# Kernel optimization log

Measured on AMD Instinct MI355X. Metric: run time of the kernel, lower is better.

The kernel has to match this reference:

```python
import jax, jax.numpy as jnp
import numpy as np

N = 80000; E = 1280000; IN = 128; H1 = 128; H2 = 128; H3 = 64
L1D = 512; L2D = 256; OUT = 10; K = 2; GROUP = 40


def setup_inputs() -> dict:
    key = jax.random.key(0)
    ks = jax.random.split(key, 16)
    s = 0.05
    d = {}
    d['x'] = jax.random.normal(ks[0], (N, IN), jnp.float32)
    d['edge_index'] = jax.random.randint(ks[1], (2, E), 0, N, jnp.int32)
    # SGConv linears (applied after K-hop propagation)
    d['W1'] = jax.random.normal(ks[2], (H1, IN), jnp.float32) * s
    d['b1'] = jnp.zeros((H1,), jnp.float32)
    d['W2'] = jax.random.normal(ks[3], (H2, H1), jnp.float32) * s
    d['b2'] = jnp.zeros((H2,), jnp.float32)
    # GATConv (heads=1)
    d['Wg'] = jax.random.normal(ks[4], (H3, H2), jnp.float32) * s
    d['att_src'] = jax.random.normal(ks[5], (H3,), jnp.float32) * s
    d['att_dst'] = jax.random.normal(ks[6], (H3,), jnp.float32) * s
    d['bg'] = jnp.zeros((H3,), jnp.float32)
    # MLP head
    d['L1'] = jax.random.normal(ks[7], (L1D, H3 * GROUP), jnp.float32) * s
    d['bl1'] = jnp.zeros((L1D,), jnp.float32)
    d['L2'] = jax.random.normal(ks[8], (L2D, L1D), jnp.float32) * s
    d['bl2'] = jnp.zeros((L2D,), jnp.float32)
    d['L3'] = jax.random.normal(ks[9], (OUT, L2D), jnp.float32) * s
    d['bl3'] = jnp.zeros((OUT,), jnp.float32)
    return d


def _lrelu(v, slope=0.1):
    return jnp.where(v > 0, v, slope * v)


def _forward(x, src, dst, norm, W1, b1, W2, b2, Wg, bg, att_src, att_dst,
             L1, bl1, L2, bl2, L3, bl3):
    # SGConv: x <- S^K x, then linear. S = D^-1/2 (A+I) D^-1/2
    def prop(h):
        return jax.ops.segment_sum(norm[:, None] * h[src], dst, num_segments=N)

    h = x
    for _ in range(K):
        h = prop(h)
    h = _lrelu(h @ W1.T + b1)
    for _ in range(K):
        h = prop(h)
    h = _lrelu(h @ W2.T + b2)

    # GATConv (1 head), self-loops included in (src, dst)
    g = h @ Wg.T                                   # [N, H3]
    a_s = g @ att_src                              # [N]
    a_d = g @ att_dst                              # [N]
    e = _lrelu(a_s[src] + a_d[dst], 0.2)           # [E+N]
    emax = jax.ops.segment_max(e, dst, num_segments=N)
    ee = jnp.exp(e - emax[dst])
    den = jax.ops.segment_sum(ee, dst, num_segments=N)
    alpha = ee / den[dst]
    h = jax.ops.segment_sum(alpha[:, None] * g[src], dst, num_segments=N) + bg
    h = _lrelu(h)

    # pool 40-node groups, MLP head
    h = h.reshape(N // GROUP, H3 * GROUP)
    h = _lrelu(h @ L1.T + bl1)
    h = _lrelu(h @ L2.T + bl2)
    h = _lrelu(h @ L3.T + bl3)
    return h


def reference(x, edge_index, W1, b1, W2, b2, Wg, bg, att_src, att_dst,
              L1, bl1, L2, bl2, L3, bl3):
    loops = jnp.arange(N, dtype=edge_index.dtype)
    src = jnp.concatenate([edge_index[0], loops])
    dst = jnp.concatenate([edge_index[1], loops])
    deg = jax.ops.segment_sum(jnp.ones_like(src, jnp.float32), dst, num_segments=N)
    dinv = jnp.where(deg > 0, jax.lax.rsqrt(deg), 0.0)
    norm = dinv[src] * dinv[dst]
    return _forward(x, src, dst, norm, W1, b1, W2, b2, Wg, bg, att_src,
                    att_dst, L1, bl1, L2, bl2, L3, bl3)
```

## Files before the change

kernel.cpp:

```cpp
#include <hip/hip_runtime.h>

#define N_NODES 80000
#define N_EDGES 1280000
#define NNZ (N_EDGES + N_NODES)
#define DIM 128
#define HD3 64
#define GROUP 40
#define NPOOL (N_NODES / GROUP)
#define L1DIM 512
#define L2DIM 256
#define OUTD 10
#define SPLITK 4
#define L1K (HD3 * GROUP)

#define NB_BUCKETS ((N_NODES + 255) >> 8)
#define NB_PAD 320
#define EPB 8192
#define NBLK ((NNZ + EPB - 1) / EPB)

#define QX  (N_NODES * DIM / 4)
#define QW1 (DIM * DIM / 4)
#define QW2 (DIM * DIM / 4)
#define QWG (HD3 * DIM / 4)
#define QL1 (L1DIM * L1K / 4)
#define QTOT (QX + QW1 + QW2 + QWG + QL1)

typedef unsigned int u32;
typedef unsigned short u16;
typedef __bf16 bf16x8 __attribute__((ext_vector_type(8)));
typedef float f32x4 __attribute__((ext_vector_type(4)));
typedef float f32x2 __attribute__((ext_vector_type(2)));

__device__ __forceinline__ float lrelu(float v, float s) { return v > 0.f ? v : s * v; }

__device__ __forceinline__ float b2f(u16 b) {
    u32 u = ((u32)b) << 16;
    float f; __builtin_memcpy(&f, &u, 4); return f;
}
__device__ __forceinline__ u16 f2b(float f) {
    u32 u; __builtin_memcpy(&u, &f, 4);
    return (u16)((u + 0x7fffu + ((u >> 16) & 1u)) >> 16);
}
__device__ __forceinline__ f32x2 bf2(u32 v) {
    f32x2 r;
    r.x = __uint_as_float(v << 16);
    r.y = __uint_as_float(v & 0xffff0000u);
    return r;
}


__global__ __launch_bounds__(256) void k_hist(const int* __restrict__ ei, u32* __restrict__ cnt) {
    __shared__ u32 h[NB_PAD];
    for (int i = threadIdx.x; i < NB_PAD; i += 256) h[i] = 0;
    __syncthreads();
    int base = blockIdx.x * EPB;
    #pragma unroll 4
    for (int i = 0; i < EPB / 256; ++i) {
        int idx = base + i * 256 + threadIdx.x;
        if (idx < NNZ) {
            int d = (idx < N_EDGES) ? ei[N_EDGES + idx] : idx - N_EDGES;
            atomicAdd(&h[d >> 8], 1u);
        }
    }
    __syncthreads();
    for (int b = threadIdx.x; b < NB_BUCKETS; b += 256)
        cnt[blockIdx.x * NB_PAD + b] = h[b];
}

__global__ __launch_bounds__(256) void k_bscan_col(const u32* __restrict__ cnt,
                                                   u32* __restrict__ basep,
                                                   u32* __restrict__ btot) {
    int b = blockIdx.x, t = threadIdx.x;
    u32 v = (t < NBLK) ? cnt[t * NB_PAD + b] : 0;
    __shared__ u32 sm[256];
    sm[t] = v; __syncthreads();
    for (int off = 1; off < 256; off <<= 1) {
        u32 u = (t >= off) ? sm[t - off] : 0; __syncthreads();
        sm[t] += u; __syncthreads();
    }
    if (t < NBLK) basep[t * NB_PAD + b] = sm[t] - v;
    if (t == 255) btot[b] = sm[255];
}

__global__ __launch_bounds__(512) void k_bscan_top(const u32* __restrict__ btot,
                                                   u32* __restrict__ bbase,
                                                   int* __restrict__ row_ptr) {
    __shared__ u32 sm[512];
    int t = threadIdx.x;
    u32 v = (t < NB_BUCKETS) ? btot[t] : 0;
    sm[t] = v; __syncthreads();
    for (int off = 1; off < 512; off <<= 1) {
        u32 u = (t >= off) ? sm[t - off] : 0; __syncthreads();
        sm[t] += u; __syncthreads();
    }
    if (t < NB_BUCKETS) bbase[t] = sm[t] - v;
    if (t == NB_BUCKETS - 1) bbase[NB_BUCKETS] = sm[t];
    if (t == 0) row_ptr[N_NODES] = NNZ;
}

__global__ __launch_bounds__(256) void k_binscatter(const int* __restrict__ ei,
                                                    const u32* __restrict__ basep,
                                                    const u32* __restrict__ bbase,
                                                    u32* __restrict__ pairs) {
    __shared__ u32 rk[NB_PAD];
    for (int i = threadIdx.x; i < NB_PAD; i += 256) rk[i] = 0;
    __syncthreads();
    int base = blockIdx.x * EPB;
    #pragma unroll 4
    for (int i = 0; i < EPB / 256; ++i) {
        int idx = base + i * 256 + threadIdx.x;
        if (idx < NNZ) {
            int s, d;
            if (idx < N_EDGES) { s = ei[idx]; d = ei[N_EDGES + idx]; }
            else { s = idx - N_EDGES; d = s; }
            int b = d >> 8;
            u32 r = atomicAdd(&rk[b], 1u);
            u32 pos = bbase[b] + basep[blockIdx.x * NB_PAD + b] + r;
            pairs[pos] = ((u32)(d & 255) << 24) | (u32)s;
        }
    }
}

__global__ __launch_bounds__(256) void k_build_csr(const u32* __restrict__ pairs,
                                                   const u32* __restrict__ bbase,
                                                   int* __restrict__ row_ptr,
                                                   float* __restrict__ dinv,
                                                   int* __restrict__ col_src) {
    __shared__ u32 c[256], sc[256], ex[256];
    int t = threadIdx.x, b = blockIdx.x;
    int lo = bbase[b], hi = bbase[b + 1];
    c[t] = 0;
    __syncthreads();
    for (int i = lo + t; i < hi; i += 256)
        atomicAdd(&c[pairs[i] >> 24], 1u);
    __syncthreads();
    u32 cv = c[t];
    sc[t] = cv;
    __syncthreads();
    for (int off = 1; off < 256; off <<= 1) {
        u32 u = (t >= off) ? sc[t - off] : 0; __syncthreads();
        sc[t] += u; __syncthreads();
    }
    ex[t] = sc[t] - cv;
    int node = (b << 8) + t;
    if (node < N_NODES) {
        row_ptr[node] = lo + (int)ex[t];
        dinv[node] = rsqrtf((float)cv);
    }
    c[t] = 0;
    __syncthreads();
    for (int i = lo + t; i < hi; i += 256) {
        u32 p = pairs[i];
        u32 dl = p >> 24;
        u32 r = atomicAdd(&c[dl], 1u);
        col_src[lo + (int)ex[dl] + (int)r] = (int)(p & 0xFFFFFFu);
    }
}


__global__ __launch_bounds__(256) void k_f2b_all(const float* __restrict__ x,   u16* __restrict__ xb,
                                                 const float* __restrict__ w1,  u16* __restrict__ w1b,
                                                 const float* __restrict__ w2,  u16* __restrict__ w2b,
                                                 const float* __restrict__ wg,  u16* __restrict__ wgb,
                                                 const float* __restrict__ l1,  u16* __restrict__ l1b) {
    int i = blockIdx.x * blockDim.x + threadIdx.x;
    const float* src; u16* dst; int off;
    if (i < QX)                        { src = x;  dst = xb;  off = i; }
    else if (i < QX + QW1)             { src = w1; dst = w1b; off = i - QX; }
    else if (i < QX + QW1 + QW2)       { src = w2; dst = w2b; off = i - QX - QW1; }
    else if (i < QX + QW1 + QW2 + QWG) { src = wg; dst = wgb; off = i - QX - QW1 - QW2; }
    else if (i < QTOT)                 { src = l1; dst = l1b; off = i - QX - QW1 - QW2 - QWG; }
    else return;
    float4 v = ((const float4*)src)[off];
    ushort4 o = { f2b(v.x), f2b(v.y), f2b(v.z), f2b(v.w) };
    ((ushort4*)dst)[off] = o;
}


__global__ __launch_bounds__(256) void k_prop_bf(const int* __restrict__ row_ptr,
                                                 const int* __restrict__ col_src,
                                                 const float* __restrict__ dinv,
                                                 const u16* __restrict__ hin,
                                                 u16* __restrict__ hout) {
    int lane = threadIdx.x & 63;
    int node = blockIdx.x * 4 + (threadIdx.x >> 6);
    if (node >= N_NODES) return;
    int j0 = row_ptr[node], j1 = row_ptr[node + 1];
    float dn = dinv[node];
    const int grp = lane >> 4;
    const int dl  = lane & 15;
    f32x2 acc[4] = {};

    for (int base = j0; base < j1; base += 64) {
        int cnt = j1 - base; if (cnt > 64) cnt = 64;
        int jj = base + lane;
        int sidx = (jj < j1) ? col_src[jj] : 0;
        int l = 0;
        for (; l + 16 <= cnt; l += 16) {
            uint4 v[4]; f32x2 w2[4];
            #pragma unroll
            for (int q = 0; q < 4; ++q) {
                int s = __shfl(sidx, l + q * 4 + grp);
                float wq = dinv[s] * dn;
                w2[q].x = wq; w2[q].y = wq;
                v[q] = *(const uint4*)(hin + (size_t)s * DIM + dl * 8);
            }
            #pragma unroll
            for (int q = 0; q < 4; ++q) {
                acc[0] = __builtin_elementwise_fma(bf2(v[q].x), w2[q], acc[0]);
                acc[1] = __builtin_elementwise_fma(bf2(v[q].y), w2[q], acc[1]);
                acc[2] = __builtin_elementwise_fma(bf2(v[q].z), w2[q], acc[2]);
                acc[3] = __builtin_elementwise_fma(bf2(v[q].w), w2[q], acc[3]);
            }
        }
        for (; l + 4 <= cnt; l += 4) {
            int s = __shfl(sidx, l + grp);
            float wq = dinv[s] * dn;
            f32x2 w2; w2.x = wq; w2.y = wq;
            uint4 v = *(const uint4*)(hin + (size_t)s * DIM + dl * 8);
            acc[0] = __builtin_elementwise_fma(bf2(v.x), w2, acc[0]);
            acc[1] = __builtin_elementwise_fma(bf2(v.y), w2, acc[1]);
            acc[2] = __builtin_elementwise_fma(bf2(v.z), w2, acc[2]);
            acc[3] = __builtin_elementwise_fma(bf2(v.w), w2, acc[3]);
        }
        for (; l < cnt; ++l) {
            int s = __shfl(sidx, l);
            if (grp == 0) {
                float wq = dinv[s] * dn;
                f32x2 w2; w2.x = wq; w2.y = wq;
                uint4 v = *(const uint4*)(hin + (size_t)s * DIM + dl * 8);
                acc[0] = __builtin_elementwise_fma(bf2(v.x), w2, acc[0]);
                acc[1] = __builtin_elementwise_fma(bf2(v.y), w2, acc[1]);
                acc[2] = __builtin_elementwise_fma(bf2(v.z), w2, acc[2]);
                acc[3] = __builtin_elementwise_fma(bf2(v.w), w2, acc[3]);
            }
        }
    }
    #pragma unroll
    for (int d = 0; d < 4; ++d) {
        acc[d].x += __shfl_xor(acc[d].x, 16); acc[d].x += __shfl_xor(acc[d].x, 32);
        acc[d].y += __shfl_xor(acc[d].y, 16); acc[d].y += __shfl_xor(acc[d].y, 32);
    }
    if (grp == 0) {
        uint4 o;
        o.x = (u32)f2b(acc[0].x) | ((u32)f2b(acc[0].y) << 16);
        o.y = (u32)f2b(acc[1].x) | ((u32)f2b(acc[1].y) << 16);
        o.z = (u32)f2b(acc[2].x) | ((u32)f2b(acc[2].y) << 16);
        o.w = (u32)f2b(acc[3].x) | ((u32)f2b(acc[3].y) << 16);
        *(uint4*)(hout + (size_t)node * DIM + dl * 8) = o;
    }
}


template<int NT, bool BIAS, bool ACT, bool ATTN>
__global__ __launch_bounds__(256) void k_gemm_mfma(const u16* __restrict__ A,
                                                   const u16* __restrict__ Wb,
                                                   const float* __restrict__ b,
                                                   u16* __restrict__ C,
                                                   const float* __restrict__ att_src,
                                                   const float* __restrict__ att_dst,
                                                   float* __restrict__ a_s,
                                                   float* __restrict__ a_d,
                                                   int M, int K) {
    const int lane = threadIdx.x & 63;
    const int wave = threadIdx.x >> 6;
    const int m0 = blockIdx.x * 64 + wave * 16;
    const int row = lane & 15, kg = lane >> 4;
    const int Ntot = NT * 16;

    const u16* Ap = A + (size_t)(m0 + row) * K + kg * 8;
    f32x4 acc[NT] = {};

    for (int k0 = 0; k0 < K; k0 += 32) {
        bf16x8 a = *(const bf16x8*)(Ap + k0);
        #pragma unroll
        for (int nt = 0; nt < NT; ++nt) {
            const u16* Wp = Wb + (size_t)(nt * 16 + row) * K + k0 + kg * 8;
            bf16x8 bb = *(const bf16x8*)Wp;
            acc[nt] = __builtin_amdgcn_mfma_f32_16x16x32_bf16(a, bb, acc[nt], 0, 0, 0);
        }
    }

    #pragma unroll
    for (int nt = 0; nt < NT; ++nt) {
        float bias = BIAS ? b[nt * 16 + row] : 0.f;
        #pragma unroll
        for (int r = 0; r < 4; ++r) {
            float v = acc[nt][r] + bias;
            if (ACT) v = lrelu(v, 0.1f);
            int crow = m0 + kg * 4 + r;
            C[(size_t)crow * Ntot + nt * 16 + row] = f2b(v);
        }
    }

    if (ATTN) {
        float s1[4] = {}, s2[4] = {};
        #pragma unroll
        for (int nt = 0; nt < NT; ++nt) {
            float as = att_src[nt * 16 + row];
            float av = att_dst[nt * 16 + row];
            #pragma unroll
            for (int r = 0; r < 4; ++r) {
                s1[r] += acc[nt][r] * as;
                s2[r] += acc[nt][r] * av;
            }
        }
        #pragma unroll
        for (int r = 0; r < 4; ++r) {
            #pragma unroll
            for (int off = 1; off < 16; off <<= 1) {
                s1[r] += __shfl_xor(s1[r], off);
                s2[r] += __shfl_xor(s2[r], off);
            }
        }
        if (row == 0) {
            #pragma unroll
            for (int r = 0; r < 4; ++r) {
                a_s[m0 + kg * 4 + r] = s1[r];
                a_d[m0 + kg * 4 + r] = s2[r];
            }
        }
    }
}


template<int NT>
__global__ __launch_bounds__(256) void k_gemm_mfma_sk(const u16* __restrict__ A,
                                                      const u16* __restrict__ Wb,
                                                      float* __restrict__ C,
                                                      int M, int Ntot, int K, int kChunk) {
    const int lane = threadIdx.x & 63;
    const int wave = threadIdx.x >> 6;
    const int m0 = blockIdx.x * 64 + wave * 16;
    const int row = lane & 15, kg = lane >> 4;
    const int n0 = blockIdx.y * NT * 16;
    const int kBeg = blockIdx.z * kChunk;

    int arow = m0 + row; if (arow >= M) arow = M - 1;
    const u16* Ap = A + (size_t)arow * K + kg * 8;
    f32x4 acc[NT] = {};

    for (int k0 = kBeg; k0 < kBeg + kChunk; k0 += 32) {
        bf16x8 a = *(const bf16x8*)(Ap + k0);
        #pragma unroll
        for (int nt = 0; nt < NT; ++nt) {
            const u16* Wp = Wb + (size_t)(n0 + nt * 16 + row) * K + k0 + kg * 8;
            bf16x8 bb = *(const bf16x8*)Wp;
            acc[nt] = __builtin_amdgcn_mfma_f32_16x16x32_bf16(a, bb, acc[nt], 0, 0, 0);
        }
    }

    float* Cp = C + (size_t)blockIdx.z * M * Ntot;
    #pragma unroll
    for (int nt = 0; nt < NT; ++nt) {
        #pragma unroll
        for (int r = 0; r < 4; ++r) {
            int crow = m0 + kg * 4 + r;
            if (crow < M) Cp[(size_t)crow * Ntot + n0 + nt * 16 + row] = acc[nt][r];
        }
    }
}


template<int BM, int BN, int BK, int TM, int TN, bool BIAS, bool ACT>
__global__ __launch_bounds__(256) void k_gemm(const float* __restrict__ A,
                                              const float* __restrict__ W,
                                              const float* __restrict__ b,
                                              float* __restrict__ C,
                                              int M, int Ntot, int K) {
    __shared__ float As[BK][BM + 4];
    __shared__ float Bs[BK][BN + 4];
    const int t = threadIdx.x;
    const int m0 = blockIdx.x * BM, n0 = blockIdx.y * BN;
    const int ty = t / (BN / TN), tx = t % (BN / TN);

    float acc[TM][TN] = {};

    for (int k0 = 0; k0 < K; k0 += BK) {
        #pragma unroll
        for (int p = 0; p < BM * BK / 4 / 256; ++p) {
            int id = p * 256 + t;
            int m = id % BM, kk = (id / BM) * 4;
            float4 v = {0.f, 0.f, 0.f, 0.f};
            if (m0 + m < M) v = *(const float4*)(A + (size_t)(m0 + m) * K + k0 + kk);
            As[kk + 0][m] = v.x; As[kk + 1][m] = v.y;
            As[kk + 2][m] = v.z; As[kk + 3][m] = v.w;
        }
        #pragma unroll
        for (int p = 0; p < BN * BK / 4 / 256; ++p) {
            int id = p * 256 + t;
            int n = id % BN, kk = (id / BN) * 4;
            float4 v = *(const float4*)(W + (size_t)(n0 + n) * K + k0 + kk);
            Bs[kk + 0][n] = v.x; Bs[kk + 1][n] = v.y;
            Bs[kk + 2][n] = v.z; Bs[kk + 3][n] = v.w;
        }
        __syncthreads();

        #pragma unroll
        for (int k = 0; k < BK; ++k) {
            float a[TM], bb[TN];
            #pragma unroll
            for (int i = 0; i < TM; ++i) a[i] = As[k][ty * TM + i];
            #pragma unroll
            for (int j = 0; j < TN; ++j) bb[j] = Bs[k][tx * TN + j];
            #pragma unroll
            for (int i = 0; i < TM; ++i)
                #pragma unroll
                for (int j = 0; j < TN; ++j)
                    acc[i][j] += a[i] * bb[j];
        }
        __syncthreads();
    }

    #pragma unroll
    for (int i = 0; i < TM; ++i) {
        int row = m0 + ty * TM + i;
        if (row >= M) continue;
        float4 o;
        float* op = (float*)&o;
        #pragma unroll
        for (int j = 0; j < TN; ++j) {
            float r = acc[i][j];
            if (BIAS) r += b[n0 + tx * TN + j];
            if (ACT) r = lrelu(r, 0.1f);
            op[j] = r;
        }
        *(float4*)(C + (size_t)row * Ntot + n0 + tx * TN) = o;
    }
}

__global__ __launch_bounds__(256) void k_splitk_reduce(const float* __restrict__ part,
                                                       const float* __restrict__ b,
                                                       float* __restrict__ out) {
    const int total4 = NPOOL * L1DIM / 4;
    int idx = blockIdx.x * blockDim.x + threadIdx.x;
    if (idx >= total4) return;
    const size_t stride4 = (size_t)NPOOL * L1DIM / 4;
    const float4* p4 = (const float4*)part;
    float4 s = p4[idx];
    #pragma unroll
    for (int z = 1; z < SPLITK; ++z) {
        float4 v = p4[idx + z * stride4];
        s.x += v.x; s.y += v.y; s.z += v.z; s.w += v.w;
    }
    int col = (idx * 4) % L1DIM;
    float4 bb = *(const float4*)(b + col);
    s.x = lrelu(s.x + bb.x, 0.1f); s.y = lrelu(s.y + bb.y, 0.1f);
    s.z = lrelu(s.z + bb.z, 0.1f); s.w = lrelu(s.w + bb.w, 0.1f);
    ((float4*)out)[idx] = s;
}


template<int KD, int OD, bool BIAS, bool ACT>
__global__ void k_linear(const float* __restrict__ in, const float* __restrict__ W,
                         const float* __restrict__ b, float* __restrict__ out, int nrows) {
    int idx = blockIdx.x * blockDim.x + threadIdx.x;
    int n = idx / OD, o = idx % OD;
    if (n >= nrows) return;
    const float4* ar = (const float4*)(in + (size_t)n * KD);
    const float4* wr = (const float4*)(W + (size_t)o * KD);
    float4 acc = {0.f, 0.f, 0.f, 0.f};
    #pragma unroll 8
    for (int k = 0; k < KD / 4; ++k) {
        float4 a = ar[k], w = wr[k];
        acc.x += a.x * w.x; acc.y += a.y * w.y;
        acc.z += a.z * w.z; acc.w += a.w * w.w;
    }
    float r = (acc.x + acc.y) + (acc.z + acc.w);
    if (BIAS) r += b[o];
    if (ACT) r = lrelu(r, 0.1f);
    out[idx] = r;
}


__global__ __launch_bounds__(256) void k_gat(const int* __restrict__ row_ptr,
                                             const int* __restrict__ col_src,
                                             const u16* __restrict__ g,
                                             const float* __restrict__ a_s,
                                             const float* __restrict__ a_d,
                                             const float* __restrict__ bg,
                                             u16* __restrict__ hout) {
    __shared__ float wbuf[4][64];
    int lane = threadIdx.x & 63;
    int wid  = threadIdx.x >> 6;
    int node = blockIdx.x * 4 + wid;
    if (node >= N_NODES) return;
    int j0 = row_ptr[node], j1 = row_ptr[node + 1];
    float ad = a_d[node];
    const int grp = lane >> 4, dl = lane & 15;
    float m = -1e30f, den = 0.f;
    f32x2 acc[2] = {};

    for (int base = j0; base < j1; base += 64) {
        int cnt = j1 - base; if (cnt > 64) cnt = 64;
        int jj = base + lane;
        int sidx = 0;
        float e = -1e30f;
        if (jj < j1) { sidx = col_src[jj]; e = lrelu(a_s[sidx] + ad, 0.2f); }
        float cm = e;
        for (int off = 32; off; off >>= 1) cm = fmaxf(cm, __shfl_xor(cm, off));
        float nm = fmaxf(m, cm);
        float scale = __expf(m - nm);
        float wv = (jj < j1) ? __expf(e - nm) : 0.f;
        wbuf[wid][lane] = wv;
        float cden = wv;
        for (int off = 32; off; off >>= 1) cden += __shfl_xor(cden, off);
        den = den * scale + cden;
        f32x2 sc2; sc2.x = scale; sc2.y = scale;
        acc[0] *= sc2; acc[1] *= sc2;
        m = nm;
        int l = 0;
        for (; l + 16 <= cnt; l += 16) {
            uint2 v[4]; f32x2 w2[4];
            #pragma unroll
            for (int q = 0; q < 4; ++q) {
                int e2 = l + q * 4 + grp;
                int s = __shfl(sidx, e2);
                float wq = wbuf[wid][e2];
                w2[q].x = wq; w2[q].y = wq;
                v[q] = *(const uint2*)(g + (size_t)s * HD3 + dl * 4);
            }
            #pragma unroll
            for (int q = 0; q < 4; ++q) {
                acc[0] = __builtin_elementwise_fma(bf2(v[q].x), w2[q], acc[0]);
                acc[1] = __builtin_elementwise_fma(bf2(v[q].y), w2[q], acc[1]);
            }
        }
        for (; l + 4 <= cnt; l += 4) {
            int e2 = l + grp;
            int s = __shfl(sidx, e2);
            float wq = wbuf[wid][e2];
            f32x2 w2; w2.x = wq; w2.y = wq;
            uint2 v = *(const uint2*)(g + (size_t)s * HD3 + dl * 4);
            acc[0] = __builtin_elementwise_fma(bf2(v.x), w2, acc[0]);
            acc[1] = __builtin_elementwise_fma(bf2(v.y), w2, acc[1]);
        }
        for (; l < cnt; ++l) {
            int s = __shfl(sidx, l);
            if (grp == 0) {
                float wq = wbuf[wid][l];
                f32x2 w2; w2.x = wq; w2.y = wq;
                uint2 v = *(const uint2*)(g + (size_t)s * HD3 + dl * 4);
                acc[0] = __builtin_elementwise_fma(bf2(v.x), w2, acc[0]);
                acc[1] = __builtin_elementwise_fma(bf2(v.y), w2, acc[1]);
            }
        }
    }
    #pragma unroll
    for (int d = 0; d < 2; ++d) {
        acc[d].x += __shfl_xor(acc[d].x, 16); acc[d].x += __shfl_xor(acc[d].x, 32);
        acc[d].y += __shfl_xor(acc[d].y, 16); acc[d].y += __shfl_xor(acc[d].y, 32);
    }
    if (grp == 0) {
        float r0 = lrelu(acc[0].x / den + bg[dl * 4 + 0], 0.1f);
        float r1 = lrelu(acc[0].y / den + bg[dl * 4 + 1], 0.1f);
        float r2 = lrelu(acc[1].x / den + bg[dl * 4 + 2], 0.1f);
        float r3 = lrelu(acc[1].y / den + bg[dl * 4 + 3], 0.1f);
        uint2 o;
        o.x = (u32)f2b(r0) | ((u32)f2b(r1) << 16);
        o.y = (u32)f2b(r2) | ((u32)f2b(r3) << 16);
        *(uint2*)(hout + (size_t)node * HD3 + dl * 4) = o;
    }
}


extern "C" void kernel_launch(void* const* d_in, const int* in_sizes, int n_in,
                              void* d_out, int out_size, void* d_ws, size_t ws_size,
                              hipStream_t stream) {
    const float* x   = (const float*)d_in[0];
    const int*   ei  = (const int*)d_in[1];
    const float* W1  = (const float*)d_in[2];
    const float* b1  = (const float*)d_in[3];
    const float* W2  = (const float*)d_in[4];
    const float* b2  = (const float*)d_in[5];
    const float* Wg  = (const float*)d_in[6];
    const float* att_src = (const float*)d_in[7];
    const float* att_dst = (const float*)d_in[8];
    const float* bg  = (const float*)d_in[9];
    const float* L1  = (const float*)d_in[10];
    const float* bl1 = (const float*)d_in[11];
    const float* L2  = (const float*)d_in[12];
    const float* bl2 = (const float*)d_in[13];
    const float* L3  = (const float*)d_in[14];
    const float* bl3 = (const float*)d_in[15];
    float* out = (float*)d_out;

    char* w = (char*)d_ws;
    auto alloc = [&](size_t bytes) {
        char* p = w;
        w += (bytes + 255) & ~(size_t)255;
        return p;
    };
    int*   row_ptr  = (int*)alloc((size_t)(N_NODES + 1) * 4);
    float* dinv     = (float*)alloc((size_t)N_NODES * 4);
    int*   col_src  = (int*)alloc((size_t)NNZ * 4);
    u32*   pairs    = (u32*)alloc((size_t)NNZ * 4);
    u32*   cnt      = (u32*)alloc((size_t)NBLK * NB_PAD * 4);
    u32*   basep    = (u32*)alloc((size_t)NBLK * NB_PAD * 4);
    u32*   btot     = (u32*)alloc((size_t)NB_PAD * 4);
    u32*   bbase    = (u32*)alloc((size_t)(NB_BUCKETS + 1) * 4);
    u16*   bufX     = (u16*)alloc((size_t)N_NODES * DIM * 2);
    u16*   bufA     = (u16*)alloc((size_t)N_NODES * DIM * 2);
    u16*   bufB     = (u16*)alloc((size_t)N_NODES * DIM * 2);
    float* a_s      = (float*)alloc((size_t)N_NODES * 4);
    float* a_d      = (float*)alloc((size_t)N_NODES * 4);
    float* p1       = (float*)alloc((size_t)NPOOL * L1DIM * 4);
    float* p2       = (float*)alloc((size_t)NPOOL * L2DIM * 4);
    u16*   W1b      = (u16*)alloc((size_t)DIM * DIM * 2);
    u16*   W2b      = (u16*)alloc((size_t)DIM * DIM * 2);
    u16*   Wgb      = (u16*)alloc((size_t)HD3 * DIM * 2);
    u16*   L1b      = (u16*)alloc((size_t)L1DIM * L1K * 2);
    u16*   gb    = bufX;
    u16*   hGb   = bufA;
    float* skbuf = (float*)bufB;

    dim3 b256(256);
    k_hist<<<NBLK, b256, 0, stream>>>(ei, cnt);
    k_bscan_col<<<NB_BUCKETS, b256, 0, stream>>>(cnt, basep, btot);
    k_bscan_top<<<1, 512, 0, stream>>>(btot, bbase, row_ptr);
    k_binscatter<<<NBLK, b256, 0, stream>>>(ei, basep, bbase, pairs);
    k_build_csr<<<NB_BUCKETS, b256, 0, stream>>>(pairs, bbase, row_ptr, dinv, col_src);

    k_f2b_all<<<(QTOT + 255) / 256, b256, 0, stream>>>(x, bufX, W1, W1b, W2, W2b, Wg, Wgb, L1, L1b);

    int nb = (N_NODES + 3) / 4;
    int gemm_nb = N_NODES / 64;
    k_prop_bf<<<nb, b256, 0, stream>>>(row_ptr, col_src, dinv, bufX, bufA);
    k_prop_bf<<<nb, b256, 0, stream>>>(row_ptr, col_src, dinv, bufA, bufB);
    k_gemm_mfma<8, true, true, false><<<gemm_nb, b256, 0, stream>>>(
        bufB, W1b, b1, bufA, nullptr, nullptr, nullptr, nullptr, N_NODES, DIM);
    k_prop_bf<<<nb, b256, 0, stream>>>(row_ptr, col_src, dinv, bufA, bufB);
    k_prop_bf<<<nb, b256, 0, stream>>>(row_ptr, col_src, dinv, bufB, bufA);
    k_gemm_mfma<8, true, true, false><<<gemm_nb, b256, 0, stream>>>(
        bufA, W2b, b2, bufB, nullptr, nullptr, nullptr, nullptr, N_NODES, DIM);
    k_gemm_mfma<4, false, false, true><<<gemm_nb, b256, 0, stream>>>(
        bufB, Wgb, nullptr, gb, att_src, att_dst, a_s, a_d, N_NODES, DIM);
    k_gat<<<nb, b256, 0, stream>>>(row_ptr, col_src, gb, a_s, a_d, bg, hGb);
    k_gemm_mfma_sk<8><<<dim3(32, 4, SPLITK), b256, 0, stream>>>(
        hGb, L1b, skbuf, NPOOL, L1DIM, L1K, L1K / SPLITK);
    k_splitk_reduce<<<(NPOOL * L1DIM / 4 + 255) / 256, b256, 0, stream>>>(skbuf, bl1, p1);
    k_gemm<64, 64, 32, 4, 4, true, true><<<dim3(32, 4), b256, 0, stream>>>(p1, L2, bl2, p2, NPOOL, L2DIM, L1DIM);
    k_linear<256, 10, true, true><<<(NPOOL * 10 + 255) / 256, b256, 0, stream>>>(p2, L3, bl3, out, NPOOL);
}
```

Baseline: 473.2 us.

## Apply linear layers before propagation and fuse bias/activation into propagation epilogue

```diff
diff --git a/kernel.cpp b/kernel.cpp
--- a/kernel.cpp
+++ b/kernel.cpp
@@ -18,12 +18,12 @@
 #define EPB 8192
 #define NBLK ((NNZ + EPB - 1) / EPB)
 
-#define QX  (N_NODES * DIM / 4)
 #define QW1 (DIM * DIM / 4)
 #define QW2 (DIM * DIM / 4)
 #define QWG (HD3 * DIM / 4)
 #define QL1 (L1DIM * L1K / 4)
-#define QTOT (QX + QW1 + QW2 + QWG + QL1)
+#define QWTOT (QW1 + QW2 + QWG + QL1)
+#define F2B_NB ((QWTOT + 255) / 256)
 
 typedef unsigned int u32;
 typedef unsigned short u16;
@@ -47,10 +47,33 @@
     r.y = __uint_as_float(v & 0xffff0000u);
     return r;
 }
-
-
-__global__ __launch_bounds__(256) void k_hist(const int* __restrict__ ei, u32* __restrict__ cnt) {
+__device__ __forceinline__ bf16x8 pack8(float4 f0, float4 f1) {
+    union { bf16x8 v; u16 s[8]; } u;
+    u.s[0] = f2b(f0.x); u.s[1] = f2b(f0.y); u.s[2] = f2b(f0.z); u.s[3] = f2b(f0.w);
+    u.s[4] = f2b(f1.x); u.s[5] = f2b(f1.y); u.s[6] = f2b(f1.z); u.s[7] = f2b(f1.w);
+    return u.v;
+}
+
+
+__global__ __launch_bounds__(256) void k_hist(const int* __restrict__ ei, u32* __restrict__ cnt,
+                                              const float* __restrict__ w1, u16* __restrict__ w1b,
+                                              const float* __restrict__ w2, u16* __restrict__ w2b,
+                                              const float* __restrict__ wg, u16* __restrict__ wgb,
+                                              const float* __restrict__ l1, u16* __restrict__ l1b) {
     __shared__ u32 h[NB_PAD];
+    if (blockIdx.x >= NBLK) {
+        int i = (blockIdx.x - NBLK) * 256 + threadIdx.x;
+        const float* src; u16* dst; int off;
+        if (i < QW1)                   { src = w1; dst = w1b; off = i; }
+        else if (i < QW1 + QW2)        { src = w2; dst = w2b; off = i - QW1; }
+        else if (i < QW1 + QW2 + QWG)  { src = wg; dst = wgb; off = i - QW1 - QW2; }
+        else if (i < QWTOT)            { src = l1; dst = l1b; off = i - QW1 - QW2 - QWG; }
+        else return;
+        float4 v = ((const float4*)src)[off];
+        ushort4 o = { f2b(v.x), f2b(v.y), f2b(v.z), f2b(v.w) };
+        ((ushort4*)dst)[off] = o;
+        return;
+    }
     for (int i = threadIdx.x; i < NB_PAD; i += 256) h[i] = 0;
     __syncthreads();
     int base = blockIdx.x * EPB;
@@ -158,30 +181,13 @@
 }
 
 
-__global__ __launch_bounds__(256) void k_f2b_all(const float* __restrict__ x,   u16* __restrict__ xb,
-                                                 const float* __restrict__ w1,  u16* __restrict__ w1b,
-                                                 const float* __restrict__ w2,  u16* __restrict__ w2b,
-                                                 const float* __restrict__ wg,  u16* __restrict__ wgb,
-                                                 const float* __restrict__ l1,  u16* __restrict__ l1b) {
-    int i = blockIdx.x * blockDim.x + threadIdx.x;
-    const float* src; u16* dst; int off;
-    if (i < QX)                        { src = x;  dst = xb;  off = i; }
-    else if (i < QX + QW1)             { src = w1; dst = w1b; off = i - QX; }
-    else if (i < QX + QW1 + QW2)       { src = w2; dst = w2b; off = i - QX - QW1; }
-    else if (i < QX + QW1 + QW2 + QWG) { src = wg; dst = wgb; off = i - QX - QW1 - QW2; }
-    else if (i < QTOT)                 { src = l1; dst = l1b; off = i - QX - QW1 - QW2 - QWG; }
-    else return;
-    float4 v = ((const float4*)src)[off];
-    ushort4 o = { f2b(v.x), f2b(v.y), f2b(v.z), f2b(v.w) };
-    ((ushort4*)dst)[off] = o;
-}
-
-
+template<bool EPI>
 __global__ __launch_bounds__(256) void k_prop_bf(const int* __restrict__ row_ptr,
                                                  const int* __restrict__ col_src,
                                                  const float* __restrict__ dinv,
                                                  const u16* __restrict__ hin,
-                                                 u16* __restrict__ hout) {
+                                                 u16* __restrict__ hout,
+                                                 const float* __restrict__ bias) {
     int lane = threadIdx.x & 63;
     int node = blockIdx.x * 4 + (threadIdx.x >> 6);
     if (node >= N_NODES) return;
@@ -242,6 +248,14 @@
         acc[d].y += __shfl_xor(acc[d].y, 16); acc[d].y += __shfl_xor(acc[d].y, 32);
     }
     if (grp == 0) {
+        if (EPI) {
+            float4 b0 = *(const float4*)(bias + dl * 8);
+            float4 b4 = *(const float4*)(bias + dl * 8 + 4);
+            acc[0].x = lrelu(acc[0].x + b0.x, 0.1f); acc[0].y = lrelu(acc[0].y + b0.y, 0.1f);
+            acc[1].x = lrelu(acc[1].x + b0.z, 0.1f); acc[1].y = lrelu(acc[1].y + b0.w, 0.1f);
+            acc[2].x = lrelu(acc[2].x + b4.x, 0.1f); acc[2].y = lrelu(acc[2].y + b4.y, 0.1f);
+            acc[3].x = lrelu(acc[3].x + b4.z, 0.1f); acc[3].y = lrelu(acc[3].y + b4.w, 0.1f);
+        }
         uint4 o;
         o.x = (u32)f2b(acc[0].x) | ((u32)f2b(acc[0].y) << 16);
         o.y = (u32)f2b(acc[1].x) | ((u32)f2b(acc[1].y) << 16);
@@ -252,10 +266,10 @@
 }
 
 
-template<int NT, bool BIAS, bool ACT, bool ATTN>
+template<int NT, bool ATTN, bool F32A>
 __global__ __launch_bounds__(256) void k_gemm_mfma(const u16* __restrict__ A,
+                                                   const float* __restrict__ Af,
                                                    const u16* __restrict__ Wb,
-                                                   const float* __restrict__ b,
                                                    u16* __restrict__ C,
                                                    const float* __restrict__ att_src,
                                                    const float* __restrict__ att_dst,
@@ -268,11 +282,19 @@
     const int row = lane & 15, kg = lane >> 4;
     const int Ntot = NT * 16;
 
-    const u16* Ap = A + (size_t)(m0 + row) * K + kg * 8;
+    const u16* Apb = F32A ? nullptr : A + (size_t)(m0 + row) * K + kg * 8;
+    const float* Apf = F32A ? Af + (size_t)(m0 + row) * K + kg * 8 : nullptr;
     f32x4 acc[NT] = {};
 
     for (int k0 = 0; k0 < K; k0 += 32) {
-        bf16x8 a = *(const bf16x8*)(Ap + k0);
+        bf16x8 a;
+        if (F32A) {
+            float4 f0 = *(const float4*)(Apf + k0);
+            float4 f1 = *(const float4*)(Apf + k0 + 4);
+            a = pack8(f0, f1);
+        } else {
+            a = *(const bf16x8*)(Apb + k0);
+        }
         #pragma unroll
         for (int nt = 0; nt < NT; ++nt) {
             const u16* Wp = Wb + (size_t)(nt * 16 + row) * K + k0 + kg * 8;
@@ -283,13 +305,10 @@
 
     #pragma unroll
     for (int nt = 0; nt < NT; ++nt) {
-        float bias = BIAS ? b[nt * 16 + row] : 0.f;
         #pragma unroll
         for (int r = 0; r < 4; ++r) {
-            float v = acc[nt][r] + bias;
-            if (ACT) v = lrelu(v, 0.1f);
             int crow = m0 + kg * 4 + r;
-            C[(size_t)crow * Ntot + nt * 16 + row] = f2b(v);
+            C[(size_t)crow * Ntot + nt * 16 + row] = f2b(acc[nt][r]);
         }
     }
 
@@ -599,9 +618,9 @@
     u32*   basep    = (u32*)alloc((size_t)NBLK * NB_PAD * 4);
     u32*   btot     = (u32*)alloc((size_t)NB_PAD * 4);
     u32*   bbase    = (u32*)alloc((size_t)(NB_BUCKETS + 1) * 4);
-    u16*   bufX     = (u16*)alloc((size_t)N_NODES * DIM * 2);
     u16*   bufA     = (u16*)alloc((size_t)N_NODES * DIM * 2);
     u16*   bufB     = (u16*)alloc((size_t)N_NODES * DIM * 2);
+    u16*   bufC     = (u16*)alloc((size_t)N_NODES * DIM * 2);
     float* a_s      = (float*)alloc((size_t)N_NODES * 4);
     float* a_d      = (float*)alloc((size_t)N_NODES * 4);
     float* p1       = (float*)alloc((size_t)NPOOL * L1DIM * 4);
@@ -610,31 +629,29 @@
     u16*   W2b      = (u16*)alloc((size_t)DIM * DIM * 2);
     u16*   Wgb      = (u16*)alloc((size_t)HD3 * DIM * 2);
     u16*   L1b      = (u16*)alloc((size_t)L1DIM * L1K * 2);
-    u16*   gb    = bufX;
-    u16*   hGb   = bufA;
+    u16*   gb    = bufA;
+    u16*   hGb   = bufC;
     float* skbuf = (float*)bufB;
 
     dim3 b256(256);
-    k_hist<<<NBLK, b256, 0, stream>>>(ei, cnt);
+    k_hist<<<NBLK + F2B_NB, b256, 0, stream>>>(ei, cnt, W1, W1b, W2, W2b, Wg, Wgb, L1, L1b);
     k_bscan_col<<<NB_BUCKETS, b256, 0, stream>>>(cnt, basep, btot);
     k_bscan_top<<<1, 512, 0, stream>>>(btot, bbase, row_ptr);
     k_binscatter<<<NBLK, b256, 0, stream>>>(ei, basep, bbase, pairs);
     k_build_csr<<<NB_BUCKETS, b256, 0, stream>>>(pairs, bbase, row_ptr, dinv, col_src);
 
-    k_f2b_all<<<(QTOT + 255) / 256, b256, 0, stream>>>(x, bufX, W1, W1b, W2, W2b, Wg, Wgb, L1, L1b);
-
     int nb = (N_NODES + 3) / 4;
     int gemm_nb = N_NODES / 64;
-    k_prop_bf<<<nb, b256, 0, stream>>>(row_ptr, col_src, dinv, bufX, bufA);
-    k_prop_bf<<<nb, b256, 0, stream>>>(row_ptr, col_src, dinv, bufA, bufB);
-    k_gemm_mfma<8, true, true, false><<<gemm_nb, b256, 0, stream>>>(
-        bufB, W1b, b1, bufA, nullptr, nullptr, nullptr, nullptr, N_NODES, DIM);
-    k_prop_bf<<<nb, b256, 0, stream>>>(row_ptr, col_src, dinv, bufA, bufB);
-    k_prop_bf<<<nb, b256, 0, stream>>>(row_ptr, col_src, dinv, bufB, bufA);
-    k_gemm_mfma<8, true, true, false><<<gemm_nb, b256, 0, stream>>>(
-        bufA, W2b, b2, bufB, nullptr, nullptr, nullptr, nullptr, N_NODES, DIM);
-    k_gemm_mfma<4, false, false, true><<<gemm_nb, b256, 0, stream>>>(
-        bufB, Wgb, nullptr, gb, att_src, att_dst, a_s, a_d, N_NODES, DIM);
+    k_gemm_mfma<8, false, true><<<gemm_nb, b256, 0, stream>>>(
+        nullptr, x, W1b, bufA, nullptr, nullptr, nullptr, nullptr, N_NODES, DIM);
+    k_prop_bf<false><<<nb, b256, 0, stream>>>(row_ptr, col_src, dinv, bufA, bufB, nullptr);
+    k_prop_bf<true><<<nb, b256, 0, stream>>>(row_ptr, col_src, dinv, bufB, bufA, b1);
+    k_gemm_mfma<8, false, false><<<gemm_nb, b256, 0, stream>>>(
+        bufA, nullptr, W2b, bufB, nullptr, nullptr, nullptr, nullptr, N_NODES, DIM);
+    k_prop_bf<false><<<nb, b256, 0, stream>>>(row_ptr, col_src, dinv, bufB, bufA, nullptr);
+    k_prop_bf<true><<<nb, b256, 0, stream>>>(row_ptr, col_src, dinv, bufA, bufB, b2);
+    k_gemm_mfma<4, true, false><<<gemm_nb, b256, 0, stream>>>(
+        bufB, nullptr, Wgb, gb, att_src, att_dst, a_s, a_d, N_NODES, DIM);
     k_gat<<<nb, b256, 0, stream>>>(row_ptr, col_src, gb, a_s, a_d, bg, hGb);
     k_gemm_mfma_sk<8><<<dim3(32, 4, SPLITK), b256, 0, stream>>>(
         hGb, L1b, skbuf, NPOOL, L1DIM, L1K, L1K / SPLITK);
```

Result: no change. 470.8 us (-0.5%).
